# Kernel optimization log

Hardware: AMD Instinct MI355X
Metric: run time of the kernel (lower is better)

## Reference

```python
import jax, jax.numpy as jnp
import numpy as np

LN_EPS = 1e-5

def setup_inputs() -> dict:
    key = jax.random.key(0)
    ks = jax.random.split(key, 12)
    B, S, D = 4, 2048, 1024
    s = 1.0 / np.sqrt(D)
    return {
        "query": jax.random.normal(ks[0], (B, S, D), jnp.float32),
        "key_in": jax.random.normal(ks[1], (B, S, D), jnp.float32),
        "value": jax.random.normal(ks[2], (B, S, D), jnp.float32),
        "Wq": jax.random.normal(ks[3], (D, D), jnp.float32) * s,
        "bq": jax.random.normal(ks[4], (D,), jnp.float32) * s,
        "Wk": jax.random.normal(ks[5], (D, D), jnp.float32) * s,
        "bk": jax.random.normal(ks[6], (D,), jnp.float32) * s,
        "Wv": jax.random.normal(ks[7], (D, D), jnp.float32) * s,
        "bv": jax.random.normal(ks[8], (D,), jnp.float32) * s,
        "gamma": jnp.ones((D,), jnp.float32),
        "beta": jnp.zeros((D,), jnp.float32),
    }

def reference(query, key_in, value, Wq, bq, Wk, bk, Wv, bv, gamma, beta):
    # Linear projections (torch Linear: x @ W^T + b; here W stored as [in,out])
    q = jnp.einsum('bsd,df->bsf', query, Wq) + bq
    k = jnp.einsum('bsd,df->bsf', key_in, Wk) + bk
    v = jnp.einsum('bsd,df->bsf', value, Wv) + bv
    # Attention: note NO 1/sqrt(d) scaling, single head (faithful to source)
    attn = jnp.einsum('bqd,bkd->bqk', q, k)          # [B,S,S]
    probs = jax.nn.softmax(attn, axis=-1)
    result = jnp.einsum('bqk,bkd->bqd', probs, v)     # [B,S,D]
    # Residual + LayerNorm
    x = result + query
    mu = jnp.mean(x, axis=-1, keepdims=True)
    var = jnp.mean((x - mu) ** 2, axis=-1, keepdims=True)
    return (x - mu) * jax.lax.rsqrt(var + LN_EPS) * gamma + beta
```

## Files before the change

kernel.cpp:

```cpp
#include <hip/hip_runtime.h>
#include <hip/hip_bf16.h>
#include <cstdint>


typedef unsigned short u16;
typedef unsigned int   u32;
typedef _Float16 f16;
typedef f16   f16x8  __attribute__((ext_vector_type(8)));
typedef f16   f16x4  __attribute__((ext_vector_type(4)));
typedef float f32x4  __attribute__((ext_vector_type(4)));

#define DEV __device__ __forceinline__

DEV void gld_lds16(const f16* g, char* l){
  __builtin_amdgcn_global_load_lds(
      (const __attribute__((address_space(1))) u32*)(uintptr_t)g,
      (__attribute__((address_space(3))) u32*)(u32)(uintptr_t)l, 16, 0, 0);
}

DEV int swz_lid(){
  int lid = (blockIdx.z * gridDim.y + blockIdx.y) * gridDim.x + blockIdx.x;
  int cpx = (gridDim.x * gridDim.y * gridDim.z) >> 3;
  return (lid & 7) * cpx + (lid >> 3);
}

#define MFMA_(av, bv, ci, cj) \
  acc[ci][cj] = __builtin_amdgcn_mfma_f32_16x16x32_f16(av, bv, acc[ci][cj], 0, 0, 0)

template<bool MORE>
DEV void ktile_body(const f16* (&src)[8], char* bufc, char* stash,
                    int ob0, int ob1, int rA, int rB, int sk0, int sk1,
                    f32x4 (&acc)[8][4])
{
  f16x8 a0[4], a1[4], b0[2], b1[2], b2[2], b3[2];

  if (MORE){ gld_lds16(src[0], stash + 0 + ob0); src[0] += 64; }
  if (MORE) asm volatile("s_waitcnt vmcnt(5)\ns_barrier" ::: "memory");
  else      asm volatile("s_waitcnt vmcnt(4)\ns_barrier" ::: "memory");
#pragma unroll
  for (int i = 0; i < 4; i++) a0[i] = *(const f16x8*)(bufc + (i << 12) + rA + sk0);
  b0[0] = *(const f16x8*)(bufc + 32768 +    0 + rB + sk0);
  b0[1] = *(const f16x8*)(bufc + 32768 + 8192 + rB + sk0);
  __builtin_amdgcn_s_setprio(1);
#pragma unroll
  for (int i = 0; i < 4; i++){ MFMA_(a0[i], b0[0], i, 0); MFMA_(a0[i], b0[1], i, 1); }
  __builtin_amdgcn_s_setprio(0);

  if (MORE){ gld_lds16(src[1], stash + 0 + ob1); src[1] += 64; }
#pragma unroll
  for (int i = 0; i < 4; i++) a1[i] = *(const f16x8*)(bufc + (i << 12) + rA + sk1);
  b1[0] = *(const f16x8*)(bufc + 32768 +    0 + rB + sk1);
  b1[1] = *(const f16x8*)(bufc + 32768 + 8192 + rB + sk1);
  __builtin_amdgcn_s_setprio(1);
#pragma unroll
  for (int i = 0; i < 4; i++){ MFMA_(a1[i], b1[0], i, 0); MFMA_(a1[i], b1[1], i, 1); }
  __builtin_amdgcn_s_setprio(0);

  if (MORE){ gld_lds16(src[2], stash + 32768 + ob0); src[2] += 64; }
  if (MORE) asm volatile("s_waitcnt vmcnt(3)\ns_barrier" ::: "memory");
  else      asm volatile("s_waitcnt vmcnt(0)\ns_barrier" ::: "memory");
  b2[0] = *(const f16x8*)(bufc + 49152 +    0 + rB + sk0);
  b2[1] = *(const f16x8*)(bufc + 49152 + 8192 + rB + sk0);
  __builtin_amdgcn_s_setprio(1);
#pragma unroll
  for (int i = 0; i < 4; i++){ MFMA_(a0[i], b2[0], i, 2); MFMA_(a0[i], b2[1], i, 3); }
  __builtin_amdgcn_s_setprio(0);

  if (MORE){ gld_lds16(src[3], stash + 32768 + ob1); src[3] += 64; }
  b3[0] = *(const f16x8*)(bufc + 49152 +    0 + rB + sk1);
  b3[1] = *(const f16x8*)(bufc + 49152 + 8192 + rB + sk1);
  __builtin_amdgcn_s_setprio(1);
#pragma unroll
  for (int i = 0; i < 4; i++){ MFMA_(a1[i], b3[0], i, 2); MFMA_(a1[i], b3[1], i, 3); }
  __builtin_amdgcn_s_setprio(0);

  if (MORE){ gld_lds16(src[4], stash + 16384 + ob0); src[4] += 64; }
#pragma unroll
  for (int i = 0; i < 4; i++) a0[i] = *(const f16x8*)(bufc + 16384 + (i << 12) + rA + sk0);
  __builtin_amdgcn_s_setprio(1);
#pragma unroll
  for (int i = 0; i < 4; i++){ MFMA_(a0[i], b0[0], 4 + i, 0); MFMA_(a0[i], b0[1], 4 + i, 1); }
  __builtin_amdgcn_s_setprio(0);

  if (MORE){ gld_lds16(src[5], stash + 16384 + ob1); src[5] += 64; }
#pragma unroll
  for (int i = 0; i < 4; i++) a1[i] = *(const f16x8*)(bufc + 16384 + (i << 12) + rA + sk1);
  __builtin_amdgcn_s_setprio(1);
#pragma unroll
  for (int i = 0; i < 4; i++){ MFMA_(a1[i], b1[0], 4 + i, 0); MFMA_(a1[i], b1[1], 4 + i, 1); }
  __builtin_amdgcn_s_setprio(0);

  if (MORE){ gld_lds16(src[6], stash + 49152 + ob0); src[6] += 64; }
  __builtin_amdgcn_s_setprio(1);
#pragma unroll
  for (int i = 0; i < 4; i++){ MFMA_(a0[i], b2[0], 4 + i, 2); MFMA_(a0[i], b2[1], 4 + i, 3); }
  __builtin_amdgcn_s_setprio(0);

  if (MORE){ gld_lds16(src[7], stash + 49152 + ob1); src[7] += 64; }
  __builtin_amdgcn_s_setprio(1);
#pragma unroll
  for (int i = 0; i < 4; i++){ MFMA_(a1[i], b3[0], 4 + i, 2); MFMA_(a1[i], b3[1], 4 + i, 3); }
  __builtin_amdgcn_s_setprio(0);
}

DEV void gemm_core(const f16* __restrict__ A, int lda,
                   const f16* __restrict__ B, int ldb,
                   int nt, char* smem, f32x4 (&acc)[8][4])
{
  const int tid  = threadIdx.x;
  const int lane = tid & 63;
  const int wv   = tid >> 6;
  const int wm   = wv >> 2, wn = wv & 3;
  const int lr   = lane & 15, lq = lane >> 4;

  const int ob0 = tid * 16;
  const int ob1 = ob0 + 8192;
  const int r0  = ob0 >> 7, r1 = ob1 >> 7;
  const int sl0 = ((ob0 >> 4) & 7) ^ (r0 & 7);
  const int sl1 = ((ob1 >> 4) & 7) ^ (r1 & 7);
  const f16* src[8];
  src[0] = A + (size_t)r0 * lda + sl0 * 8;
  src[1] = A + (size_t)r1 * lda + sl1 * 8;
  src[2] = B + (size_t)r0 * ldb + sl0 * 8;
  src[3] = B + (size_t)r1 * ldb + sl1 * 8;
  src[4] = A + (size_t)(128 + r0) * lda + sl0 * 8;
  src[5] = A + (size_t)(128 + r1) * lda + sl1 * 8;
  src[6] = B + (size_t)(128 + r0) * ldb + sl0 * 8;
  src[7] = B + (size_t)(128 + r1) * ldb + sl1 * 8;

  const int rA  = (wm * 16 + lr) << 7;
  const int rB  = (wn * 16 + lr) << 7;
  const int sk0 = ((lq ^ (lane & 7)) << 4);
  const int sk1 = (((4 | lq) ^ (lane & 7)) << 4);

#pragma unroll
  for (int i = 0; i < 8; i++)
#pragma unroll
    for (int j = 0; j < 4; j++) acc[i][j] = (f32x4){0.f, 0.f, 0.f, 0.f};

  gld_lds16(src[0], smem +     0 + ob0); src[0] += 64;
  gld_lds16(src[1], smem +     0 + ob1); src[1] += 64;
  gld_lds16(src[2], smem + 32768 + ob0); src[2] += 64;
  gld_lds16(src[3], smem + 32768 + ob1); src[3] += 64;
  gld_lds16(src[4], smem + 16384 + ob0); src[4] += 64;
  gld_lds16(src[5], smem + 16384 + ob1); src[5] += 64;
  gld_lds16(src[6], smem + 49152 + ob0); src[6] += 64;
  gld_lds16(src[7], smem + 49152 + ob1); src[7] += 64;

  for (int t = 0; t < nt - 1; ++t){
    char* bufc  = smem + ((t & 1) << 16);
    char* stash = smem + (((t & 1) ^ 1) << 16);
    ktile_body<true>(src, bufc, stash, ob0, ob1, rA, rB, sk0, sk1, acc);
  }
  {
    char* bufc  = smem + (((nt - 1) & 1) << 16);
    char* stash = smem + ((((nt - 1) & 1) ^ 1) << 16);
    ktile_body<false>(src, bufc, stash, ob0, ob1, rA, rB, sk0, sk1, acc);
  }
}

__global__ __launch_bounds__(512, 2) void proj8p(
    const f16* __restrict__ xq, const f16* __restrict__ xk, const f16* __restrict__ xv,
    const f16* __restrict__ wq, const f16* __restrict__ wk, const f16* __restrict__ wv,
    const float* __restrict__ bq, const float* __restrict__ bk, const float* __restrict__ bv,
    f16* __restrict__ oq, f16* __restrict__ ok, f16* __restrict__ ovT)
{
  __shared__ char smem[131072];
  const int s  = swz_lid();
  const int bx = s & 3, by = (s >> 2) & 31, z = s >> 7;
  const int m0 = by * 256, n0 = bx * 256;
  const f16* A = (z == 0 ? xq : z == 1 ? xk : xv) + (size_t)m0 * 1024;
  const f16* B = (z == 0 ? wq : z == 1 ? wk : wv) + (size_t)n0 * 1024;
  const float* bias = (z == 0 ? bq : z == 1 ? bk : bv);

  f32x4 acc[8][4];
  gemm_core(A, 1024, B, 1024, 16, smem, acc);

  const int lane = threadIdx.x & 63;
  const int wv_  = threadIdx.x >> 6;
  const int wm = wv_ >> 2, wn = wv_ & 3;
  const int lr = lane & 15, rj = (lane >> 4) * 4;

  if (z < 2){
    f16* o = z ? ok : oq;
#pragma unroll
    for (int i = 0; i < 8; i++)
#pragma unroll
      for (int j = 0; j < 4; j++){
        int row = m0 + i * 32 + wm * 16 + rj;
        int col = n0 + j * 64 + wn * 16 + lr;
        float bvl = bias[col];
#pragma unroll
        for (int r = 0; r < 4; r++)
          o[(size_t)(row + r) * 1024 + col] = (f16)(acc[i][j][r] + bvl);
      }
  } else {
#pragma unroll
    for (int i = 0; i < 8; i++)
#pragma unroll
      for (int j = 0; j < 4; j++){
        int row = m0 + i * 32 + wm * 16 + rj;
        int col = n0 + j * 64 + wn * 16 + lr;
        float bvl = bias[col];
        f16x4 tv;
#pragma unroll
        for (int r = 0; r < 4; r++) tv[r] = (f16)(acc[i][j][r] + bvl);
        *(f16x4*)(ovT + (size_t)col * 8192 + row) = tv;
      }
  }
}

__global__ __launch_bounds__(512, 2) void qk8p(
    const f16* __restrict__ q, const f16* __restrict__ k, float* __restrict__ Sout)
{
  __shared__ char smem[131072];
  const int s  = swz_lid();
  const int bx = s & 7, by = (s >> 3) & 7, z = s >> 6;
  const int m0 = by * 256, n0 = bx * 256;
  const f16* A = q + (size_t)z * 2048 * 1024 + (size_t)m0 * 1024;
  const f16* B = k + (size_t)z * 2048 * 1024 + (size_t)n0 * 1024;

  f32x4 acc[8][4];
  gemm_core(A, 1024, B, 1024, 16, smem, acc);

  const int lane = threadIdx.x & 63;
  const int wv_  = threadIdx.x >> 6;
  const int wm = wv_ >> 2, wn = wv_ & 3;
  const int lr = lane & 15, rj = (lane >> 4) * 4;
  float* o = Sout + (size_t)z * 2048 * 2048;
#pragma unroll
  for (int i = 0; i < 8; i++)
#pragma unroll
    for (int j = 0; j < 4; j++){
      int row = m0 + i * 32 + wm * 16 + rj;
      int col = n0 + j * 64 + wn * 16 + lr;
#pragma unroll
      for (int r = 0; r < 4; r++)
        o[(size_t)(row + r) * 2048 + col] = acc[i][j][r];
    }
}

__global__ __launch_bounds__(512, 2) void pv8p(
    const f16* __restrict__ P, const f16* __restrict__ vT, f16* __restrict__ O)
{
  __shared__ char smem[131072];
  const int s  = swz_lid();
  const int bx = s & 3, by = (s >> 2) & 7, z = s >> 5;
  const int zb = z >> 1, h = z & 1;
  const int m0 = by * 256, n0 = bx * 256;
  const f16* A = P  + (size_t)zb * 2048 * 2048 + (size_t)m0 * 2048 + h * 1024;
  const f16* B = vT + (size_t)n0 * 8192 + (size_t)zb * 2048 + h * 1024;

  f32x4 acc[8][4];
  gemm_core(A, 2048, B, 8192, 16, smem, acc);

  const int lane = threadIdx.x & 63;
  const int wv_  = threadIdx.x >> 6;
  const int wm = wv_ >> 2, wn = wv_ & 3;
  const int lr = lane & 15, rj = (lane >> 4) * 4;
  f16* o = O + (size_t)h * 8388608 + (size_t)zb * 2048 * 1024;
#pragma unroll
  for (int i = 0; i < 8; i++)
#pragma unroll
    for (int j = 0; j < 4; j++){
      int row = m0 + i * 32 + wm * 16 + rj;
      int col = n0 + j * 64 + wn * 16 + lr;
#pragma unroll
      for (int r = 0; r < 4; r++)
        o[(size_t)(row + r) * 1024 + col] = (f16)acc[i][j][r];
    }
}

__global__ __launch_bounds__(256) void cvt3_f32_f16(
    const float* __restrict__ x0, const float* __restrict__ x1, const float* __restrict__ x2,
    f16* __restrict__ y0, f16* __restrict__ y1, f16* __restrict__ y2){
  const int z = blockIdx.y;
  const float* x = z == 0 ? x0 : z == 1 ? x1 : x2;
  f16* y = z == 0 ? y0 : z == 1 ? y1 : y2;
  int i = (blockIdx.x * 256 + threadIdx.x) * 8;
  float4 a = *(const float4*)(x + i);
  float4 b = *(const float4*)(x + i + 4);
  f16x8 v;
  v[0]=(f16)a.x; v[1]=(f16)a.y; v[2]=(f16)a.z; v[3]=(f16)a.w;
  v[4]=(f16)b.x; v[5]=(f16)b.y; v[6]=(f16)b.z; v[7]=(f16)b.w;
  *(f16x8*)(y + i) = v;
}

__global__ __launch_bounds__(256) void transpose3_cvt_w(
    const float* __restrict__ W0, const float* __restrict__ W1, const float* __restrict__ W2,
    f16* __restrict__ T0, f16* __restrict__ T1, f16* __restrict__ T2, int D){
  const int z = blockIdx.z;
  const float* W = z == 0 ? W0 : z == 1 ? W1 : W2;
  f16* T = z == 0 ? T0 : z == 1 ? T1 : T2;
  __shared__ float t[32][33];
  int tx = threadIdx.x & 31, ty = threadIdx.x >> 5;
  int bx = blockIdx.x * 32, by = blockIdx.y * 32;
#pragma unroll
  for (int j = 0; j < 4; j++) t[ty + j*8][tx] = W[(size_t)(by + ty + j*8) * D + bx + tx];
  __syncthreads();
#pragma unroll
  for (int j = 0; j < 4; j++){
    float v = t[tx][ty + j*8];
    T[(size_t)(bx + ty + j*8) * D + by + tx] = (f16)v;
  }
}

__global__ __launch_bounds__(256) void softmax_rows(const float* __restrict__ S, f16* __restrict__ P){
  const int row  = blockIdx.x * 4 + (threadIdx.x >> 6);
  const int lane = threadIdx.x & 63;
  const float* x = S + (size_t)row * 2048 + lane * 32;
  float v[32];
  float m = -3.4e38f;
#pragma unroll
  for (int c = 0; c < 8; c++){
    float4 t = *(const float4*)(x + c * 4);
    v[c*4+0] = t.x; v[c*4+1] = t.y; v[c*4+2] = t.z; v[c*4+3] = t.w;
    m = fmaxf(m, fmaxf(fmaxf(t.x, t.y), fmaxf(t.z, t.w)));
  }
#pragma unroll
  for (int o = 32; o; o >>= 1) m = fmaxf(m, __shfl_xor(m, o));
  float ssum = 0.f;
#pragma unroll
  for (int j = 0; j < 32; j++){ v[j] = __expf(v[j] - m); ssum += v[j]; }
#pragma unroll
  for (int o = 32; o; o >>= 1) ssum += __shfl_xor(ssum, o);
  float inv = 1.f / ssum;
  f16* p = P + (size_t)row * 2048 + lane * 32;
#pragma unroll
  for (int c = 0; c < 4; c++){
    f16x8 ov;
#pragma unroll
    for (int j = 0; j < 8; j++) ov[j] = (f16)(v[c*8+j] * inv);
    *(f16x8*)(p + c * 8) = ov;
  }
}

DEV float wred_sum(float v){
#pragma unroll
  for (int o = 32; o; o >>= 1) v += __shfl_xor(v, o);
  return v;
}

__global__ __launch_bounds__(256) void resid_ln2(const f16* __restrict__ O0,
                                                 const f16* __restrict__ O1,
                                                 const float* __restrict__ query,
                                                 const float* __restrict__ gamma,
                                                 const float* __restrict__ beta,
                                                 float* __restrict__ out){
  const int row = blockIdx.x;
  const int tid = threadIdx.x;
  const size_t base = (size_t)row * 1024 + tid * 4;
  f16x4 o4 = *(const f16x4*)(O0 + base);
  f16x4 p4 = *(const f16x4*)(O1 + base);
  float4 q4 = *(const float4*)(query + base);
  float x[4] = {(float)o4[0] + (float)p4[0] + q4.x,
                (float)o4[1] + (float)p4[1] + q4.y,
                (float)o4[2] + (float)p4[2] + q4.z,
                (float)o4[3] + (float)p4[3] + q4.w};
  float s = 0.f, ss = 0.f;
#pragma unroll
  for (int j = 0; j < 4; j++){ s += x[j]; ss += x[j] * x[j]; }

  __shared__ float red[4];
  s = wred_sum(s);
  if ((tid & 63) == 0) red[tid >> 6] = s;
  __syncthreads();
  s = red[0] + red[1] + red[2] + red[3];
  ss = wred_sum(ss);
  __syncthreads();
  if ((tid & 63) == 0) red[tid >> 6] = ss;
  __syncthreads();
  ss = red[0] + red[1] + red[2] + red[3];

  float mu = s * (1.f / 1024.f);
  float var = ss * (1.f / 1024.f) - mu * mu;
  float rs = rsqrtf(var + 1e-5f);
  float4 g4 = *(const float4*)(gamma + tid * 4);
  float4 b4 = *(const float4*)(beta + tid * 4);
  float4 r;
  r.x = (x[0] - mu) * rs * g4.x + b4.x;
  r.y = (x[1] - mu) * rs * g4.y + b4.y;
  r.z = (x[2] - mu) * rs * g4.z + b4.z;
  r.w = (x[3] - mu) * rs * g4.w + b4.w;
  *(float4*)(out + base) = r;
}

extern "C" void kernel_launch(void* const* d_in, const int* in_sizes, int n_in,
                              void* d_out, int out_size, void* d_ws, size_t ws_size,
                              hipStream_t stream){
  const float* query  = (const float*)d_in[0];
  const float* key_in = (const float*)d_in[1];
  const float* value  = (const float*)d_in[2];
  const float* Wq = (const float*)d_in[3];
  const float* bq = (const float*)d_in[4];
  const float* Wk = (const float*)d_in[5];
  const float* bk = (const float*)d_in[6];
  const float* Wv = (const float*)d_in[7];
  const float* bv = (const float*)d_in[8];
  const float* gamma = (const float*)d_in[9];
  const float* beta  = (const float*)d_in[10];

  const int B = 4, S = 2048, D = 1024;
  const int M = B * S;
  const size_t MB = 1ull << 20;
  char* ws = (char*)d_ws;

  f16* qf16 = (f16*)(ws + 0);
  f16* kf16 = (f16*)(ws + 16 * MB);
  f16* vT   = (f16*)(ws + 32 * MB);
  f16* wt_q = (f16*)(ws + 48 * MB);
  f16* wt_k = (f16*)(ws + 50 * MB);
  f16* wt_v = (f16*)(ws + 52 * MB);
  f16* Obuf = (f16*)(ws + 54 * MB);
  f16* xq   = (f16*)(ws + 118 * MB);
  f16* xk   = (f16*)(ws + 134 * MB);
  f16* xv   = (f16*)(ws + 150 * MB);
  float* Sbuf = (float*)(ws + 118 * MB);
  f16*   Pbuf = (f16*)(ws + 182 * MB);

  dim3 blk(256);
  const int nElem = M * D;

  cvt3_f32_f16<<<dim3(nElem / 2048, 3), blk, 0, stream>>>(query, key_in, value, xq, xk, xv);
  transpose3_cvt_w<<<dim3(32, 32, 3), blk, 0, stream>>>(Wq, Wk, Wv, wt_q, wt_k, wt_v, D);

  proj8p<<<dim3(4, 32, 3), dim3(512), 0, stream>>>(xq, xk, xv, wt_q, wt_k, wt_v,
                                                   bq, bk, bv, qf16, kf16, vT);

  qk8p<<<dim3(8, 8, 4), dim3(512), 0, stream>>>(qf16, kf16, Sbuf);

  softmax_rows<<<M / 4, blk, 0, stream>>>(Sbuf, Pbuf);

  pv8p<<<dim3(4, 8, 8), dim3(512), 0, stream>>>(Pbuf, vT, Obuf);

  resid_ln2<<<M, blk, 0, stream>>>(Obuf, Obuf + 8388608, query, gamma, beta, (float*)d_out);
}
```

Baseline: 194.7 us.

## Fuse fp32-to-fp16 input conversion into projection GEMM A-tile loads

Removes the separate conversion kernel for query/key/value inputs. The projection GEMM now loads fp32 activations straight from global memory into registers, converts them to fp16 and writes them into the swizzled LDS stash, while the weight tiles still use direct global-to-LDS loads. This saves one kernel launch and the write and re-read of three fp16 intermediate tensors. In exchange the A loads go through registers, which may raise register pressure, and each tile waits on a full lgkmcnt drain.

```diff
diff --git a/kernel.cpp b/kernel.cpp
--- a/kernel.cpp
+++ b/kernel.cpp
@@ -22,6 +22,13 @@
   int lid = (blockIdx.z * gridDim.y + blockIdx.y) * gridDim.x + blockIdx.x;
   int cpx = (gridDim.x * gridDim.y * gridDim.z) >> 3;
   return (lid & 7) * cpx + (lid >> 3);
+}
+
+DEV f16x8 cvt8(float4 a, float4 b){
+  f16x8 v;
+  v[0]=(f16)a.x; v[1]=(f16)a.y; v[2]=(f16)a.z; v[3]=(f16)a.w;
+  v[4]=(f16)b.x; v[5]=(f16)b.y; v[6]=(f16)b.z; v[7]=(f16)b.w;
+  return v;
 }
 
 #define MFMA_(av, bv, ci, cj) \
@@ -159,8 +166,164 @@
   }
 }
 
+template<bool MORE>
+DEV void ktile_proj(const float* (&srcA)[4], const f16* (&srcB)[4],
+                    char* bufc, char* stash,
+                    int ob0, int ob1, int rA, int rB, int sk0, int sk1,
+                    f32x4 (&acc)[8][4])
+{
+  f16x8 a0[4], a1[4], b0[2], b1[2], b2[2], b3[2];
+  float4 h0a, h0b, h1a, h1b;
+  float4 g0a, g0b, g1a, g1b;
+
+  if (MORE){
+    h0a = *(const float4*)(srcA[0]); h0b = *(const float4*)(srcA[0] + 4);
+    g0a = *(const float4*)(srcA[1]); g0b = *(const float4*)(srcA[1] + 4);
+    srcA[0] += 64; srcA[1] += 64;
+    asm volatile("s_waitcnt vmcnt(4) lgkmcnt(0)\ns_barrier" ::: "memory");
+  } else {
+    asm volatile("s_waitcnt vmcnt(0) lgkmcnt(0)\ns_barrier" ::: "memory");
+  }
+#pragma unroll
+  for (int i = 0; i < 4; i++) a0[i] = *(const f16x8*)(bufc + (i << 12) + rA + sk0);
+  b0[0] = *(const f16x8*)(bufc + 32768 +    0 + rB + sk0);
+  b0[1] = *(const f16x8*)(bufc + 32768 + 8192 + rB + sk0);
+  __builtin_amdgcn_s_setprio(1);
+#pragma unroll
+  for (int i = 0; i < 4; i++){ MFMA_(a0[i], b0[0], i, 0); MFMA_(a0[i], b0[1], i, 1); }
+  __builtin_amdgcn_s_setprio(0);
+
+#pragma unroll
+  for (int i = 0; i < 4; i++) a1[i] = *(const f16x8*)(bufc + (i << 12) + rA + sk1);
+  b1[0] = *(const f16x8*)(bufc + 32768 +    0 + rB + sk1);
+  b1[1] = *(const f16x8*)(bufc + 32768 + 8192 + rB + sk1);
+  __builtin_amdgcn_s_setprio(1);
+#pragma unroll
+  for (int i = 0; i < 4; i++){ MFMA_(a1[i], b1[0], i, 0); MFMA_(a1[i], b1[1], i, 1); }
+  __builtin_amdgcn_s_setprio(0);
+
+  if (MORE){
+    *(f16x8*)(stash + ob0) = cvt8(h0a, h0b);
+    *(f16x8*)(stash + ob1) = cvt8(g0a, g0b);
+    gld_lds16(srcB[0], stash + 32768 + ob0); srcB[0] += 64;
+    gld_lds16(srcB[1], stash + 32768 + ob1); srcB[1] += 64;
+    gld_lds16(srcB[2], stash + 49152 + ob0); srcB[2] += 64;
+    gld_lds16(srcB[3], stash + 49152 + ob1); srcB[3] += 64;
+  }
+  b2[0] = *(const f16x8*)(bufc + 49152 +    0 + rB + sk0);
+  b2[1] = *(const f16x8*)(bufc + 49152 + 8192 + rB + sk0);
+  __builtin_amdgcn_s_setprio(1);
+#pragma unroll
+  for (int i = 0; i < 4; i++){ MFMA_(a0[i], b2[0], i, 2); MFMA_(a0[i], b2[1], i, 3); }
+  __builtin_amdgcn_s_setprio(0);
+
+  b3[0] = *(const f16x8*)(bufc + 49152 +    0 + rB + sk1);
+  b3[1] = *(const f16x8*)(bufc + 49152 + 8192 + rB + sk1);
+  __builtin_amdgcn_s_setprio(1);
+#pragma unroll
+  for (int i = 0; i < 4; i++){ MFMA_(a1[i], b3[0], i, 2); MFMA_(a1[i], b3[1], i, 3); }
+  __builtin_amdgcn_s_setprio(0);
+
+  if (MORE){
+    h1a = *(const float4*)(srcA[2]); h1b = *(const float4*)(srcA[2] + 4);
+    g1a = *(const float4*)(srcA[3]); g1b = *(const float4*)(srcA[3] + 4);
+    srcA[2] += 64; srcA[3] += 64;
+  }
+#pragma unroll
+  for (int i = 0; i < 4; i++) a0[i] = *(const f16x8*)(bufc + 16384 + (i << 12) + rA + sk0);
+  __builtin_amdgcn_s_setprio(1);
+#pragma unroll
+  for (int i = 0; i < 4; i++){ MFMA_(a0[i], b0[0], 4 + i, 0); MFMA_(a0[i], b0[1], 4 + i, 1); }
+  __builtin_amdgcn_s_setprio(0);
+
+#pragma unroll
+  for (int i = 0; i < 4; i++) a1[i] = *(const f16x8*)(bufc + 16384 + (i << 12) + rA + sk1);
+  __builtin_amdgcn_s_setprio(1);
+#pragma unroll
+  for (int i = 0; i < 4; i++){ MFMA_(a1[i], b1[0], 4 + i, 0); MFMA_(a1[i], b1[1], 4 + i, 1); }
+  __builtin_amdgcn_s_setprio(0);
+
+  if (MORE){
+    *(f16x8*)(stash + 16384 + ob0) = cvt8(h1a, h1b);
+    *(f16x8*)(stash + 16384 + ob1) = cvt8(g1a, g1b);
+  }
+  __builtin_amdgcn_s_setprio(1);
+#pragma unroll
+  for (int i = 0; i < 4; i++){ MFMA_(a0[i], b2[0], 4 + i, 2); MFMA_(a0[i], b2[1], 4 + i, 3); }
+  __builtin_amdgcn_s_setprio(0);
+
+  __builtin_amdgcn_s_setprio(1);
+#pragma unroll
+  for (int i = 0; i < 4; i++){ MFMA_(a1[i], b3[0], 4 + i, 2); MFMA_(a1[i], b3[1], 4 + i, 3); }
+  __builtin_amdgcn_s_setprio(0);
+}
+
+DEV void gemm_core_proj(const float* __restrict__ A, int lda,
+                        const f16* __restrict__ B, int ldb,
+                        int nt, char* smem, f32x4 (&acc)[8][4])
+{
+  const int tid  = threadIdx.x;
+  const int lane = tid & 63;
+  const int wv   = tid >> 6;
+  const int wm   = wv >> 2, wn = wv & 3;
+  const int lr   = lane & 15, lq = lane >> 4;
+
+  const int ob0 = tid * 16;
+  const int ob1 = ob0 + 8192;
+  const int r0  = ob0 >> 7, r1 = ob1 >> 7;
+  const int sl0 = ((ob0 >> 4) & 7) ^ (r0 & 7);
+  const int sl1 = ((ob1 >> 4) & 7) ^ (r1 & 7);
+  const float* srcA[4];
+  srcA[0] = A + (size_t)r0 * lda + sl0 * 8;
+  srcA[1] = A + (size_t)r1 * lda + sl1 * 8;
+  srcA[2] = A + (size_t)(128 + r0) * lda + sl0 * 8;
+  srcA[3] = A + (size_t)(128 + r1) * lda + sl1 * 8;
+  const f16* srcB[4];
+  srcB[0] = B + (size_t)r0 * ldb + sl0 * 8;
+  srcB[1] = B + (size_t)r1 * ldb + sl1 * 8;
+  srcB[2] = B + (size_t)(128 + r0) * ldb + sl0 * 8;
+  srcB[3] = B + (size_t)(128 + r1) * ldb + sl1 * 8;
+
+  const int rA  = (wm * 16 + lr) << 7;
+  const int rB  = (wn * 16 + lr) << 7;
+  const int sk0 = ((lq ^ (lane & 7)) << 4);
+  const int sk1 = (((4 | lq) ^ (lane & 7)) << 4);
+
+#pragma unroll
+  for (int i = 0; i < 8; i++)
+#pragma unroll
+    for (int j = 0; j < 4; j++) acc[i][j] = (f32x4){0.f, 0.f, 0.f, 0.f};
+
+  {
+    float4 a0 = *(const float4*)(srcA[0]), a0h = *(const float4*)(srcA[0] + 4);
+    float4 a1 = *(const float4*)(srcA[1]), a1h = *(const float4*)(srcA[1] + 4);
+    float4 a2 = *(const float4*)(srcA[2]), a2h = *(const float4*)(srcA[2] + 4);
+    float4 a3 = *(const float4*)(srcA[3]), a3h = *(const float4*)(srcA[3] + 4);
+    srcA[0] += 64; srcA[1] += 64; srcA[2] += 64; srcA[3] += 64;
+    *(f16x8*)(smem +         ob0) = cvt8(a0, a0h);
+    *(f16x8*)(smem +         ob1) = cvt8(a1, a1h);
+    *(f16x8*)(smem + 16384 + ob0) = cvt8(a2, a2h);
+    *(f16x8*)(smem + 16384 + ob1) = cvt8(a3, a3h);
+  }
+  gld_lds16(srcB[0], smem + 32768 + ob0); srcB[0] += 64;
+  gld_lds16(srcB[1], smem + 32768 + ob1); srcB[1] += 64;
+  gld_lds16(srcB[2], smem + 49152 + ob0); srcB[2] += 64;
+  gld_lds16(srcB[3], smem + 49152 + ob1); srcB[3] += 64;
+
+  for (int t = 0; t < nt - 1; ++t){
+    char* bufc  = smem + ((t & 1) << 16);
+    char* stash = smem + (((t & 1) ^ 1) << 16);
+    ktile_proj<true>(srcA, srcB, bufc, stash, ob0, ob1, rA, rB, sk0, sk1, acc);
+  }
+  {
+    char* bufc  = smem + (((nt - 1) & 1) << 16);
+    char* stash = smem + ((((nt - 1) & 1) ^ 1) << 16);
+    ktile_proj<false>(srcA, srcB, bufc, stash, ob0, ob1, rA, rB, sk0, sk1, acc);
+  }
+}
+
 __global__ __launch_bounds__(512, 2) void proj8p(
-    const f16* __restrict__ xq, const f16* __restrict__ xk, const f16* __restrict__ xv,
+    const float* __restrict__ xq, const float* __restrict__ xk, const float* __restrict__ xv,
     const f16* __restrict__ wq, const f16* __restrict__ wk, const f16* __restrict__ wv,
     const float* __restrict__ bq, const float* __restrict__ bk, const float* __restrict__ bv,
     f16* __restrict__ oq, f16* __restrict__ ok, f16* __restrict__ ovT)
@@ -169,12 +332,12 @@
   const int s  = swz_lid();
   const int bx = s & 3, by = (s >> 2) & 31, z = s >> 7;
   const int m0 = by * 256, n0 = bx * 256;
-  const f16* A = (z == 0 ? xq : z == 1 ? xk : xv) + (size_t)m0 * 1024;
-  const f16* B = (z == 0 ? wq : z == 1 ? wk : wv) + (size_t)n0 * 1024;
+  const float* A = (z == 0 ? xq : z == 1 ? xk : xv) + (size_t)m0 * 1024;
+  const f16*   B = (z == 0 ? wq : z == 1 ? wk : wv) + (size_t)n0 * 1024;
   const float* bias = (z == 0 ? bq : z == 1 ? bk : bv);
 
   f32x4 acc[8][4];
-  gemm_core(A, 1024, B, 1024, 16, smem, acc);
+  gemm_core_proj(A, 1024, B, 1024, 16, smem, acc);
 
   const int lane = threadIdx.x & 63;
   const int wv_  = threadIdx.x >> 6;
@@ -269,21 +432,6 @@
       for (int r = 0; r < 4; r++)
         o[(size_t)(row + r) * 1024 + col] = (f16)acc[i][j][r];
     }
-}
-
-__global__ __launch_bounds__(256) void cvt3_f32_f16(
-    const float* __restrict__ x0, const float* __restrict__ x1, const float* __restrict__ x2,
-    f16* __restrict__ y0, f16* __restrict__ y1, f16* __restrict__ y2){
-  const int z = blockIdx.y;
-  const float* x = z == 0 ? x0 : z == 1 ? x1 : x2;
-  f16* y = z == 0 ? y0 : z == 1 ? y1 : y2;
-  int i = (blockIdx.x * 256 + threadIdx.x) * 8;
-  float4 a = *(const float4*)(x + i);
-  float4 b = *(const float4*)(x + i + 4);
-  f16x8 v;
-  v[0]=(f16)a.x; v[1]=(f16)a.y; v[2]=(f16)a.z; v[3]=(f16)a.w;
-  v[4]=(f16)b.x; v[5]=(f16)b.y; v[6]=(f16)b.z; v[7]=(f16)b.w;
-  *(f16x8*)(y + i) = v;
 }
 
 __global__ __launch_bounds__(256) void transpose3_cvt_w(
@@ -412,19 +560,15 @@
   f16* wt_k = (f16*)(ws + 50 * MB);
   f16* wt_v = (f16*)(ws + 52 * MB);
   f16* Obuf = (f16*)(ws + 54 * MB);
-  f16* xq   = (f16*)(ws + 118 * MB);
-  f16* xk   = (f16*)(ws + 134 * MB);
-  f16* xv   = (f16*)(ws + 150 * MB);
   float* Sbuf = (float*)(ws + 118 * MB);
   f16*   Pbuf = (f16*)(ws + 182 * MB);
 
   dim3 blk(256);
-  const int nElem = M * D;
-
-  cvt3_f32_f16<<<dim3(nElem / 2048, 3), blk, 0, stream>>>(query, key_in, value, xq, xk, xv);
+
   transpose3_cvt_w<<<dim3(32, 32, 3), blk, 0, stream>>>(Wq, Wk, Wv, wt_q, wt_k, wt_v, D);
 
-  proj8p<<<dim3(4, 32, 3), dim3(512), 0, stream>>>(xq, xk, xv, wt_q, wt_k, wt_v,
+  proj8p<<<dim3(4, 32, 3), dim3(512), 0, stream>>>(query, key_in, value,
+                                                   wt_q, wt_k, wt_v,
                                                    bq, bk, bv, qf16, kf16, vT);
 
   qk8p<<<dim3(8, 8, 4), dim3(512), 0, stream>>>(qf16, kf16, Sbuf);
```

Measured after the change: 214.2 us. 1.1x slower.

## Use smaller 128x256 tiles with 32-wide K steps for projection GEMM

Applied to the files above, without the earlier changes.

Replaces the projection GEMM core with a new pipelined core using 128x256 output tiles and a 32-element K step. LDS use drops from 128KB to 48KB per block and the grid doubles to 768 blocks, with launch bounds raised to four blocks per CU. The aim is better occupancy and wave balance across the CUs for the projection stage. In exchange each block reuses less data, there are more barriers per unit of work, and the per-wave MFMA tile is smaller.

```diff
diff --git a/kernel.cpp b/kernel.cpp
--- a/kernel.cpp
+++ b/kernel.cpp
@@ -159,22 +159,92 @@
   }
 }
 
-__global__ __launch_bounds__(512, 2) void proj8p(
+template<bool MORE>
+DEV void ktile_p(const f16* (&src)[3], char* bufc, char* stash,
+                 int o, int aoff, int boff, f32x4 (&acc)[4][4])
+{
+  if (MORE){
+    gld_lds16(src[0], stash +         o); src[0] += 32;
+    gld_lds16(src[1], stash +  8192 + o); src[1] += 32;
+    gld_lds16(src[2], stash + 16384 + o); src[2] += 32;
+    asm volatile("s_waitcnt vmcnt(3)\ns_barrier" ::: "memory");
+  } else {
+    asm volatile("s_waitcnt vmcnt(0)\ns_barrier" ::: "memory");
+  }
+  f16x8 a[4], b[4];
+#pragma unroll
+  for (int i = 0; i < 4; i++) a[i] = *(const f16x8*)(bufc + aoff + i * 1024);
+#pragma unroll
+  for (int j = 0; j < 4; j++) b[j] = *(const f16x8*)(bufc + boff + j * 1024);
+  __builtin_amdgcn_s_setprio(1);
+#pragma unroll
+  for (int i = 0; i < 4; i++)
+#pragma unroll
+    for (int j = 0; j < 4; j++) MFMA_(a[i], b[j], i, j);
+  __builtin_amdgcn_s_setprio(0);
+  __builtin_amdgcn_sched_barrier(0);
+  __builtin_amdgcn_s_barrier();
+}
+
+DEV void gemm_core_p(const f16* __restrict__ A, int lda,
+                     const f16* __restrict__ B, size_t ldb,
+                     int nt, char* smem, f32x4 (&acc)[4][4])
+{
+  const int tid  = threadIdx.x;
+  const int lane = tid & 63;
+  const int wv   = tid >> 6;
+  const int wm   = wv >> 2, wn = wv & 3;
+  const int lr   = lane & 15, lq = lane >> 4;
+
+  const int o  = tid * 16;
+  const int r0 = o >> 6;
+  const int sl = ((o >> 4) & 3) ^ ((r0 >> 1) & 3);
+  const f16* src[3];
+  src[0] = A + (size_t)r0 * lda + sl * 8;
+  src[1] = B + (size_t)r0 * ldb + sl * 8;
+  src[2] = B + (size_t)(128 + r0) * ldb + sl * 8;
+
+  const int sw   = (lr >> 1) & 3;
+  const int aoff =        (wm * 64 + lr) * 64 + ((lq ^ sw) << 4);
+  const int boff = 8192 + (wn * 64 + lr) * 64 + ((lq ^ sw) << 4);
+
+#pragma unroll
+  for (int i = 0; i < 4; i++)
+#pragma unroll
+    for (int j = 0; j < 4; j++) acc[i][j] = (f32x4){0.f, 0.f, 0.f, 0.f};
+
+  gld_lds16(src[0], smem +         o); src[0] += 32;
+  gld_lds16(src[1], smem +  8192 + o); src[1] += 32;
+  gld_lds16(src[2], smem + 16384 + o); src[2] += 32;
+
+  for (int t = 0; t < nt - 1; ++t){
+    char* bufc  = smem + (t & 1) * 24576;
+    char* stash = smem + ((t & 1) ^ 1) * 24576;
+    ktile_p<true>(src, bufc, stash, o, aoff, boff, acc);
+  }
+  {
+    char* bufc  = smem + ((nt - 1) & 1) * 24576;
+    char* stash = smem + (((nt - 1) & 1) ^ 1) * 24576;
+    ktile_p<false>(src, bufc, stash, o, aoff, boff, acc);
+  }
+}
+
+__global__ __launch_bounds__(512, 4) void proj8p(
     const f16* __restrict__ xq, const f16* __restrict__ xk, const f16* __restrict__ xv,
     const f16* __restrict__ wq, const f16* __restrict__ wk, const f16* __restrict__ wv,
     const float* __restrict__ bq, const float* __restrict__ bk, const float* __restrict__ bv,
     f16* __restrict__ oq, f16* __restrict__ ok, f16* __restrict__ ovT)
 {
-  __shared__ char smem[131072];
+  __shared__ char smem[49152];
   const int s  = swz_lid();
-  const int bx = s & 3, by = (s >> 2) & 31, z = s >> 7;
-  const int m0 = by * 256, n0 = bx * 256;
+  const int bx = s & 3, by = (s >> 2) & 63, z = s >> 8;
+  const int m0 = by * 128, n0 = bx * 256;
   const f16* A = (z == 0 ? xq : z == 1 ? xk : xv) + (size_t)m0 * 1024;
   const f16* B = (z == 0 ? wq : z == 1 ? wk : wv) + (size_t)n0 * 1024;
   const float* bias = (z == 0 ? bq : z == 1 ? bk : bv);
 
-  f32x4 acc[8][4];
-  gemm_core(A, 1024, B, 1024, 16, smem, acc);
+  f32x4 acc[4][4];
+  gemm_core_p(A, 1024, B, 1024, 32, smem, acc);
 
   const int lane = threadIdx.x & 63;
   const int wv_  = threadIdx.x >> 6;
@@ -184,11 +254,11 @@
   if (z < 2){
     f16* o = z ? ok : oq;
 #pragma unroll
-    for (int i = 0; i < 8; i++)
+    for (int i = 0; i < 4; i++)
 #pragma unroll
       for (int j = 0; j < 4; j++){
-        int row = m0 + i * 32 + wm * 16 + rj;
-        int col = n0 + j * 64 + wn * 16 + lr;
+        int row = m0 + wm * 64 + i * 16 + rj;
+        int col = n0 + wn * 64 + j * 16 + lr;
         float bvl = bias[col];
 #pragma unroll
         for (int r = 0; r < 4; r++)
@@ -196,11 +266,11 @@
       }
   } else {
 #pragma unroll
-    for (int i = 0; i < 8; i++)
+    for (int i = 0; i < 4; i++)
 #pragma unroll
       for (int j = 0; j < 4; j++){
-        int row = m0 + i * 32 + wm * 16 + rj;
-        int col = n0 + j * 64 + wn * 16 + lr;
+        int row = m0 + wm * 64 + i * 16 + rj;
+        int col = n0 + wn * 64 + j * 16 + lr;
         float bvl = bias[col];
         f16x4 tv;
 #pragma unroll
@@ -424,7 +494,7 @@
   cvt3_f32_f16<<<dim3(nElem / 2048, 3), blk, 0, stream>>>(query, key_in, value, xq, xk, xv);
   transpose3_cvt_w<<<dim3(32, 32, 3), blk, 0, stream>>>(Wq, Wk, Wv, wt_q, wt_k, wt_v, D);
 
-  proj8p<<<dim3(4, 32, 3), dim3(512), 0, stream>>>(xq, xk, xv, wt_q, wt_k, wt_v,
+  proj8p<<<dim3(4, 64, 3), dim3(512), 0, stream>>>(xq, xk, xv, wt_q, wt_k, wt_v,
                                                    bq, bk, bv, qf16, kf16, vT);
 
   qk8p<<<dim3(8, 8, 4), dim3(512), 0, stream>>>(qf16, kf16, Sbuf);
```

Result: no change. 192.7 us (-1.1%).
